# Kernel tuning notes

Measured on AMD Instinct MI355X. Metric: run time of the kernel, lower is better.

Reference implementation:

```python
import jax, jax.numpy as jnp
from jax import lax
import numpy as np

C = 16          # channel_n
HID = 128       # hidden_size
FIRE_RATE = 0.5
STEP_SIZE = 1.0
B, H, W = 16, 192, 192


def setup_inputs() -> dict:
    key = jax.random.key(0)
    ks = jax.random.split(key, 8)
    return {
        "x": jax.random.uniform(ks[0], (B, C, H, W), dtype=jnp.float32),
        "w1": jax.random.normal(ks[1], (HID, 3 * C), dtype=jnp.float32) * 0.1,
        "b1": jax.random.normal(ks[2], (HID,), dtype=jnp.float32) * 0.1,
        "w2": jax.random.normal(ks[3], (HID, HID), dtype=jnp.float32) * 0.1,
        "b2": jax.random.normal(ks[4], (HID,), dtype=jnp.float32) * 0.1,
        "w3": jax.random.normal(ks[5], (C, HID), dtype=jnp.float32) * 0.1,
        "b3": jax.random.normal(ks[6], (C,), dtype=jnp.float32) * 0.1,
        "fire_noise": jax.random.uniform(ks[7], (B, 1, H, W), dtype=jnp.float32),
    }


def _living_mask(x):
    # max_pool2d(alpha, 3, stride=1, pad=1) > 0.1 on alpha channel 3
    alpha = x[:, 3:4, :, :]
    m = lax.reduce_window(alpha, -jnp.inf, lax.max,
                          (1, 1, 3, 3), (1, 1, 1, 1), 'SAME')
    return m > 0.1


def _depthwise(x, k2d):
    # k2d: (3,3); depthwise conv over all C channels with same kernel
    kern = jnp.tile(k2d[None, None, :, :], (x.shape[1], 1, 1, 1))  # (C,1,3,3)
    return lax.conv_general_dilated(
        x, kern, window_strides=(1, 1), padding='SAME',
        feature_group_count=x.shape[1],
        dimension_numbers=('NCHW', 'OIHW', 'NCHW'))


def _relu6(x):
    return jnp.clip(x, 0.0, 6.0)


def reference(x, w1, b1, w2, b2, w3, b3, fire_noise):
    pre_life = _living_mask(x)

    # perceive: identity + sobel-x + sobel-y (angle = 0)
    sx = jnp.asarray(np.outer([1, 2, 1], [-1, 0, 1]) / 8.0, dtype=x.dtype)
    sy = sx.T
    y = jnp.concatenate([x, _depthwise(x, sx), _depthwise(x, sy)], axis=1)  # (B,3C,H,W)

    # pointwise MLP (1x1 convs) with ReLU6
    h = _relu6(jnp.einsum('bchw,oc->bohw', y, w1) + b1[None, :, None, None])
    h = _relu6(jnp.einsum('bchw,oc->bohw', h, w2) + b2[None, :, None, None])
    dx = (jnp.einsum('bchw,oc->bohw', h, w3) + b3[None, :, None, None]) * STEP_SIZE

    update_mask = (fire_noise <= FIRE_RATE).astype(x.dtype)  # (B,1,H,W)
    x_new = x + dx * update_mask

    post_life = _living_mask(x_new)
    life_mask = (pre_life & post_life).astype(x.dtype)
    return x_new * life_mask
```

## Files before the change

### kernel.cpp

```cpp
#include <hip/hip_runtime.h>

typedef _Float16 half8 __attribute__((ext_vector_type(8)));
typedef _Float16 half4 __attribute__((ext_vector_type(4)));
typedef float    f32x4 __attribute__((ext_vector_type(4)));

#define WH_HALVES      26624
#define ALPHA_BYTE_OFF 53248

#define NBLOCKS  256
#define ITERS    9

__global__ __launch_bounds__(256) void prep_weights(
    const float* __restrict__ w1, const float* __restrict__ w2,
    const float* __restrict__ w3, _Float16* __restrict__ wh)
{
    int i = blockIdx.x * 256 + threadIdx.x;
    if (i >= WH_HALVES) return;
    int rem = i & 511;
    int l = rem >> 3, j = rem & 7;
    int lr = l & 15, lg = l >> 4;
    _Float16 v;
    if (i < 8192) {
        int f = i >> 9;
        int nb = f >> 1, hh = f & 1;
        int o = nb * 16 + lr, k = hh * 32 + lg * 8 + j;
        v = (k < 48) ? (_Float16)w1[o * 48 + k] : (_Float16)0.f;
    } else if (i < 24576) {
        int f = (i - 8192) >> 9;
        int nb = f >> 2, kb = f & 3;
        v = (_Float16)w2[(nb * 16 + lr) * 128 + kb * 32 + lg * 8 + j];
    } else {
        int kb = (i - 24576) >> 9;
        v = (_Float16)w3[lr * 128 + kb * 32 + lg * 8 + j];
    }
    wh[i] = v;
}

#define HALO_UNITS 1584

__device__ __forceinline__ void halo_loads(const float* __restrict__ x,
                                           int bb, int h0, int w0, int tid,
                                           float pfv[2][4])
{
#pragma unroll
    for (int k = 0; k < 2; ++k) {
        int u = tid + k * 1024;
        bool valid = (u < HALO_UNITS);
        int uu = valid ? u : 0;
        int row = uu / 264, rem = uu % 264;
        int col = rem >> 2, cq = rem & 3;
        int hh = h0 - 1 + row, ww = w0 - 1 + col;
        bool inb = valid && hh >= 0 && hh < 192 && ww >= 0 && ww < 192;
#pragma unroll
        for (int cc = 0; cc < 4; ++cc)
            pfv[k][cc] = inb ? x[(((size_t)bb * 16 + cq * 4 + cc) * 192 + hh) * 192 + ww] : 0.f;
    }
}

__device__ __forceinline__ void halo_store(_Float16* __restrict__ dst, int tid,
                                           const float pfv[2][4])
{
#pragma unroll
    for (int k = 0; k < 2; ++k) {
        int u = tid + k * 1024;
        if (u < HALO_UNITS) {
            int row = u / 264, rem = u % 264;
            int col = rem >> 2, cq = rem & 3;
            half4 hv;
#pragma unroll
            for (int cc = 0; cc < 4; ++cc) hv[cc] = (_Float16)pfv[k][cc];
            *(half4*)&dst[(row * 66 + col) * 16 + cq * 4] = hv;
        }
    }
}

__global__ __launch_bounds__(1024, 4) void ca_main(
    const float* __restrict__ x,
    const float* __restrict__ b1g, const float* __restrict__ b2g,
    const float* __restrict__ b3g,
    const float* __restrict__ fire,
    const _Float16* __restrict__ wh,
    float* __restrict__ out,
    float* __restrict__ alpha_out)
{
    __shared__ __align__(16) struct {
        _Float16 w[WH_HALVES];
        _Float16 halo[2][6][66][16];
        _Float16 h[16][2048];
        float    b1[128], b2[128], b3[16];
    } s;

    const int tid  = threadIdx.x;
    const int lane = tid & 63;
    const int wave = tid >> 6;
    const int lr = lane & 15, hi = lane >> 4;

    {
        const uint4* src = (const uint4*)wh;
        uint4* dst = (uint4*)&s.w[0];
        for (int i = tid; i < 3328; i += 1024) dst[i] = src[i];
    }
    if (tid < 128) { s.b1[tid] = b1g[tid]; s.b2[tid] = b2g[tid]; }
    if (tid < 16)  { s.b3[tid] = b3g[tid]; }

    {
        int t = blockIdx.x;
        int bb = t / 144, rem = t % 144;
        int h0 = (rem / 3) * 4, w0 = (rem % 3) * 64;
        float pfv[2][4];
        halo_loads(x, bb, h0, w0, tid, pfv);
        halo_store(&s.halo[0][0][0][0], tid, pfv);
    }
    __syncthreads();

    const half8* wf = (const half8*)s.w;
    const int swzh = ((lr >> 1) & 7) << 4;
    char* hb = (char*)&s.h[wave][0];
    const int rowb = lr * 256;

    const int px = wave * 16 + lr;
    const int prow = px >> 6, pcol = px & 63;

    for (int it = 0; it < ITERS; ++it) {
        int t = blockIdx.x + it * NBLOCKS;
        int bb = t / 144, rem = t % 144;
        int h0 = (rem / 3) * 4, w0 = (rem % 3) * 64;
        const _Float16* hal = &s.halo[it & 1][0][0][0];

        float pfv[2][4];
        const bool have_next = (it + 1 < ITERS);
        if (have_next) {
            int tn = blockIdx.x + (it + 1) * NBLOCKS;
            int bbn = tn / 144, remn = tn % 144;
            halo_loads(x, bbn, (remn / 3) * 4, (remn % 3) * 64, tid, pfv);
        }
        const float fn = fire[(((size_t)bb) * 192 + h0 + prow) * 192 + w0 + pcol];

        half8 a1[2];
        {
            const half8 vz = { (_Float16)0.f, (_Float16)0.f, (_Float16)0.f, (_Float16)0.f,
                               (_Float16)0.f, (_Float16)0.f, (_Float16)0.f, (_Float16)0.f };
            half8 tp[3][3];
#pragma unroll
            for (int dr = 0; dr < 3; ++dr)
#pragma unroll
                for (int dc = 0; dc < 3; ++dc)
                    tp[dr][dc] = *(const half8*)&hal[((prow + dr) * 66 + pcol + dc) * 16 + (hi & 1) * 8];
            half8 gxa = (tp[0][2] - tp[0][0]) + (tp[2][2] - tp[2][0]);
            half8 gxb = (tp[1][2] - tp[1][0]);
            half8 gx  = gxa + gxb + gxb;
            half8 gya = (tp[2][0] - tp[0][0]) + (tp[2][2] - tp[0][2]);
            half8 gyb = (tp[2][1] - tp[0][1]);
            half8 gy  = gya + gyb + gyb;
            const _Float16 e = (_Float16)0.125f;
            gx = gx * e;
            gy = gy * e;
            a1[0] = (hi < 2) ? tp[1][1] : gx;
            a1[1] = (hi < 2) ? gy : vz;
        }

#pragma unroll
        for (int nb = 0; nb < 8; ++nb) {
            half8 bf0 = wf[(nb * 2    ) * 64 + lane];
            half8 bf1 = wf[(nb * 2 + 1) * 64 + lane];
            f32x4 acc = *(const f32x4*)&s.b1[nb * 16 + hi * 4];
            acc = __builtin_amdgcn_mfma_f32_16x16x32_f16(bf0, a1[0], acc, 0, 0, 0);
            acc = __builtin_amdgcn_mfma_f32_16x16x32_f16(bf1, a1[1], acc, 0, 0, 0);
            half4 hv;
#pragma unroll
            for (int rr = 0; rr < 4; ++rr)
                hv[rr] = (_Float16)fminf(fmaxf(acc[rr], 0.f), 6.f);
            *(half4*)(hb + rowb + ((nb * 32 + hi * 8) ^ swzh)) = hv;
        }

        half8 a2[4];
#pragma unroll
        for (int kb = 0; kb < 4; ++kb)
            a2[kb] = *(const half8*)(hb + rowb + ((kb * 64 + hi * 16) ^ swzh));
#pragma unroll
        for (int nb = 0; nb < 8; ++nb) {
            f32x4 acc = *(const f32x4*)&s.b2[nb * 16 + hi * 4];
#pragma unroll
            for (int kb = 0; kb < 4; ++kb) {
                half8 bf = wf[1024 + (nb * 4 + kb) * 64 + lane];
                acc = __builtin_amdgcn_mfma_f32_16x16x32_f16(bf, a2[kb], acc, 0, 0, 0);
            }
            half4 hv;
#pragma unroll
            for (int rr = 0; rr < 4; ++rr)
                hv[rr] = (_Float16)fminf(fmaxf(acc[rr], 0.f), 6.f);
            *(half4*)(hb + rowb + ((nb * 32 + hi * 8) ^ swzh)) = hv;
        }

        half8 a3[4];
#pragma unroll
        for (int kb = 0; kb < 4; ++kb)
            a3[kb] = *(const half8*)(hb + rowb + ((kb * 64 + hi * 16) ^ swzh));
        f32x4 acc3 = *(const f32x4*)&s.b3[hi * 4];
#pragma unroll
        for (int kb = 0; kb < 4; ++kb) {
            half8 bf = wf[3072 + kb * 64 + lane];
            acc3 = __builtin_amdgcn_mfma_f32_16x16x32_f16(bf, a3[kb], acc3, 0, 0, 0);
        }

        {
            half4 xq = *(const half4*)&hal[((1 + prow) * 66 + 1 + pcol) * 16 + hi * 4];
            const bool upd = (fn <= 0.5f);
            size_t obase = (((size_t)bb * 16) * 192 + h0 + prow) * 192 + w0 + pcol;
#pragma unroll
            for (int rr = 0; rr < 4; ++rr) {
                int c = hi * 4 + rr;
                float xn = (float)xq[rr] + (upd ? acc3[rr] : 0.f);
                out[obase + (size_t)c * 36864] = xn;
                if (hi == 0 && rr == 3)
                    alpha_out[(((size_t)bb) * 192 + h0 + prow) * 192 + w0 + pcol] = xn;
            }
        }

        if (have_next)
            halo_store(&s.halo[(it + 1) & 1][0][0][0], tid, pfv);
        __syncthreads();
    }
}

__global__ __launch_bounds__(256) void ca_mask(
    const float* __restrict__ x,
    const float* __restrict__ alpha_new,
    float* __restrict__ out)
{
    int pix = blockIdx.x * 256 + threadIdx.x;
    int ww = pix % 192; int t = pix / 192;
    int hh = t % 192;   int bb = t / 192;
    float pre = -1e30f, post = -1e30f;
#pragma unroll
    for (int di = -1; di <= 1; ++di) {
        int nh = hh + di;
        if (nh < 0 || nh >= 192) continue;
#pragma unroll
        for (int dj = -1; dj <= 1; ++dj) {
            int nw = ww + dj;
            if (nw < 0 || nw >= 192) continue;
            pre  = fmaxf(pre,  x[(((size_t)bb * 16 + 3) * 192 + nh) * 192 + nw]);
            post = fmaxf(post, alpha_new[(((size_t)bb) * 192 + nh) * 192 + nw]);
        }
    }
    bool alive = (pre > 0.1f) && (post > 0.1f);
    if (alive) return;
#pragma unroll
    for (int c = 0; c < 16; ++c) {
        out[(((size_t)bb * 16 + c) * 192 + hh) * 192 + ww] = 0.f;
    }
}

extern "C" void kernel_launch(void* const* d_in, const int* in_sizes, int n_in,
                              void* d_out, int out_size, void* d_ws, size_t ws_size,
                              hipStream_t stream) {
    const float* x    = (const float*)d_in[0];
    const float* w1   = (const float*)d_in[1];
    const float* b1   = (const float*)d_in[2];
    const float* w2   = (const float*)d_in[3];
    const float* b2   = (const float*)d_in[4];
    const float* w3   = (const float*)d_in[5];
    const float* b3   = (const float*)d_in[6];
    const float* fire = (const float*)d_in[7];
    float* out = (float*)d_out;

    _Float16* wh     = (_Float16*)d_ws;
    float* alpha_new = (float*)((char*)d_ws + ALPHA_BYTE_OFF);

    prep_weights<<<104, 256, 0, stream>>>(w1, w2, w3, wh);
    ca_main<<<NBLOCKS, 1024, 0, stream>>>(x, b1, b2, b3, fire, wh, out, alpha_new);
    ca_mask<<<2304, 256, 0, stream>>>(x, alpha_new, out);
}
```

Baseline: 73.47 us.

## Switch MLP to 32x32x16 MFMA with in-register permlane layer handoff

Measured after the change: 69.53 us. 1.06x faster.

```diff
diff --git a/kernel.cpp b/kernel.cpp
--- a/kernel.cpp
+++ b/kernel.cpp
@@ -1,14 +1,16 @@
 #include <hip/hip_runtime.h>
 
-typedef _Float16 half8 __attribute__((ext_vector_type(8)));
-typedef _Float16 half4 __attribute__((ext_vector_type(4)));
-typedef float    f32x4 __attribute__((ext_vector_type(4)));
+typedef _Float16 half8  __attribute__((ext_vector_type(8)));
+typedef _Float16 half4  __attribute__((ext_vector_type(4)));
+typedef _Float16 half2v __attribute__((ext_vector_type(2)));
+typedef float    f32x4  __attribute__((ext_vector_type(4)));
+typedef float    f32x16 __attribute__((ext_vector_type(16)));
 
 #define WH_HALVES      26624
 #define ALPHA_BYTE_OFF 53248
 
 #define NBLOCKS  256
-#define ITERS    9
+#define NTILES   1152
 
 __global__ __launch_bounds__(256) void prep_weights(
     const float* __restrict__ w1, const float* __restrict__ w2,
@@ -16,34 +18,31 @@
 {
     int i = blockIdx.x * 256 + threadIdx.x;
     if (i >= WH_HALVES) return;
-    int rem = i & 511;
+    int f = i >> 9, rem = i & 511;
     int l = rem >> 3, j = rem & 7;
-    int lr = l & 15, lg = l >> 4;
+    int l31 = l & 31, hi = l >> 5;
     _Float16 v;
-    if (i < 8192) {
-        int f = i >> 9;
-        int nb = f >> 1, hh = f & 1;
-        int o = nb * 16 + lr, k = hh * 32 + lg * 8 + j;
-        v = (k < 48) ? (_Float16)w1[o * 48 + k] : (_Float16)0.f;
-    } else if (i < 24576) {
-        int f = (i - 8192) >> 9;
-        int nb = f >> 2, kb = f & 3;
-        v = (_Float16)w2[(nb * 16 + lr) * 128 + kb * 32 + lg * 8 + j];
+    if (f < 12) {
+        int nb = f / 3, kb = f % 3;
+        v = (_Float16)w1[(nb * 32 + l31) * 48 + kb * 16 + hi * 8 + j];
+    } else if (f < 44) {
+        int ff = f - 12, nb = ff >> 3, kb = ff & 7;
+        v = (_Float16)w2[(nb * 32 + l31) * 128 + kb * 16 + hi * 8 + j];
     } else {
-        int kb = (i - 24576) >> 9;
-        v = (_Float16)w3[lr * 128 + kb * 32 + lg * 8 + j];
+        int kb = f - 44;
+        v = (l31 < 16) ? (_Float16)w3[l31 * 128 + kb * 16 + hi * 8 + j] : (_Float16)0.f;
     }
     wh[i] = v;
 }
 
-#define HALO_UNITS 1584
+#define HALO_UNITS 2640
 
 __device__ __forceinline__ void halo_loads(const float* __restrict__ x,
                                            int bb, int h0, int w0, int tid,
-                                           float pfv[2][4])
-{
-#pragma unroll
-    for (int k = 0; k < 2; ++k) {
+                                           float pfv[3][4])
+{
+#pragma unroll
+    for (int k = 0; k < 3; ++k) {
         int u = tid + k * 1024;
         bool valid = (u < HALO_UNITS);
         int uu = valid ? u : 0;
@@ -58,10 +57,10 @@
 }
 
 __device__ __forceinline__ void halo_store(_Float16* __restrict__ dst, int tid,
-                                           const float pfv[2][4])
-{
-#pragma unroll
-    for (int k = 0; k < 2; ++k) {
+                                           const float pfv[3][4])
+{
+#pragma unroll
+    for (int k = 0; k < 3; ++k) {
         int u = tid + k * 1024;
         if (u < HALO_UNITS) {
             int row = u / 264, rem = u % 264;
@@ -72,6 +71,26 @@
             *(half4*)&dst[(row * 66 + col) * 16 + cq * 4] = hv;
         }
     }
+}
+
+__device__ __forceinline__ void make_frags(const f32x16 acc, half8* fa, half8* fb)
+{
+    unsigned P[8];
+#pragma unroll
+    for (int w = 0; w < 8; ++w) {
+        half2v pk;
+        pk[0] = (_Float16)fminf(fmaxf(acc[2 * w    ], 0.f), 6.f);
+        pk[1] = (_Float16)fminf(fmaxf(acc[2 * w + 1], 0.f), 6.f);
+        P[w] = __builtin_bit_cast(unsigned, pk);
+    }
+    asm volatile("v_permlane32_swap_b32 %0, %1" : "+v"(P[0]), "+v"(P[2]));
+    asm volatile("v_permlane32_swap_b32 %0, %1" : "+v"(P[1]), "+v"(P[3]));
+    asm volatile("v_permlane32_swap_b32 %0, %1" : "+v"(P[4]), "+v"(P[6]));
+    asm volatile("v_permlane32_swap_b32 %0, %1" : "+v"(P[5]), "+v"(P[7]));
+    union { unsigned u[4]; half8 h; } A, B;
+    A.u[0] = P[0]; A.u[1] = P[1]; A.u[2] = P[2]; A.u[3] = P[3];
+    B.u[0] = P[4]; B.u[1] = P[5]; B.u[2] = P[6]; B.u[3] = P[7];
+    *fa = A.h; *fb = B.h;
 }
 
 __global__ __launch_bounds__(1024, 4) void ca_main(
@@ -85,67 +104,70 @@
 {
     __shared__ __align__(16) struct {
         _Float16 w[WH_HALVES];
-        _Float16 halo[2][6][66][16];
-        _Float16 h[16][2048];
-        float    b1[128], b2[128], b3[16];
+        _Float16 halo[2][10][66][16];
+        __align__(64) float b1d[4][2][16];
+        __align__(64) float b2d[4][2][16];
+        __align__(64) float b3d[2][16];
     } s;
 
     const int tid  = threadIdx.x;
     const int lane = tid & 63;
     const int wave = tid >> 6;
-    const int lr = lane & 15, hi = lane >> 4;
+    const int l31 = lane & 31, hi = lane >> 5;
 
     {
         const uint4* src = (const uint4*)wh;
         uint4* dst = (uint4*)&s.w[0];
         for (int i = tid; i < 3328; i += 1024) dst[i] = src[i];
     }
-    if (tid < 128) { s.b1[tid] = b1g[tid]; s.b2[tid] = b2g[tid]; }
-    if (tid < 16)  { s.b3[tid] = b3g[tid]; }
-
+    if (tid < 128) {
+        int o = tid, nb = o >> 5, ol = o & 31;
+        int r = (ol & 3) + 4 * (ol >> 3), hd = (ol >> 2) & 1;
+        s.b1d[nb][hd][r] = b1g[o];
+        s.b2d[nb][hd][r] = b2g[o];
+    }
+    if (tid < 32) {
+        int hd = tid >> 4, r = tid & 15;
+        s.b3d[hd][r] = (r < 8) ? b3g[(r & 3) + 8 * (r >> 2) + 4 * hd] : 0.f;
+    }
     {
         int t = blockIdx.x;
-        int bb = t / 144, rem = t % 144;
-        int h0 = (rem / 3) * 4, w0 = (rem % 3) * 64;
-        float pfv[2][4];
+        int bb = t / 72, rem = t % 72;
+        int h0 = (rem / 3) * 8, w0 = (rem % 3) * 64;
+        float pfv[3][4];
         halo_loads(x, bb, h0, w0, tid, pfv);
         halo_store(&s.halo[0][0][0][0], tid, pfv);
     }
     __syncthreads();
 
     const half8* wf = (const half8*)s.w;
-    const int swzh = ((lr >> 1) & 7) << 4;
-    char* hb = (char*)&s.h[wave][0];
-    const int rowb = lr * 256;
-
-    const int px = wave * 16 + lr;
+    const int px = wave * 32 + l31;
     const int prow = px >> 6, pcol = px & 63;
 
-    for (int it = 0; it < ITERS; ++it) {
+    for (int it = 0; ; ++it) {
         int t = blockIdx.x + it * NBLOCKS;
-        int bb = t / 144, rem = t % 144;
-        int h0 = (rem / 3) * 4, w0 = (rem % 3) * 64;
+        if (t >= NTILES) break;
+        int bb = t / 72, rem = t % 72;
+        int h0 = (rem / 3) * 8, w0 = (rem % 3) * 64;
         const _Float16* hal = &s.halo[it & 1][0][0][0];
 
-        float pfv[2][4];
-        const bool have_next = (it + 1 < ITERS);
+        float pfv[3][4];
+        int tn = t + NBLOCKS;
+        const bool have_next = (tn < NTILES);
         if (have_next) {
-            int tn = blockIdx.x + (it + 1) * NBLOCKS;
-            int bbn = tn / 144, remn = tn % 144;
-            halo_loads(x, bbn, (remn / 3) * 4, (remn % 3) * 64, tid, pfv);
+            int bbn = tn / 72, remn = tn % 72;
+            halo_loads(x, bbn, (remn / 3) * 8, (remn % 3) * 64, tid, pfv);
         }
         const float fn = fire[(((size_t)bb) * 192 + h0 + prow) * 192 + w0 + pcol];
 
-        half8 a1[2];
+        half8 bs0, bs1, bs2;
         {
-            const half8 vz = { (_Float16)0.f, (_Float16)0.f, (_Float16)0.f, (_Float16)0.f,
-                               (_Float16)0.f, (_Float16)0.f, (_Float16)0.f, (_Float16)0.f };
             half8 tp[3][3];
 #pragma unroll
             for (int dr = 0; dr < 3; ++dr)
 #pragma unroll
                 for (int dc = 0; dc < 3; ++dc)
-                    tp[dr][dc] = *(const half8*)&hal[((prow + dr) * 66 + pcol + dc) * 16 + (hi & 1) * 8];
+                    tp[dr][dc] = *(const half8*)&hal[((prow + dr) * 66 + pcol + dc) * 16 + hi * 8];
             half8 gxa = (tp[0][2] - tp[0][0]) + (tp[2][2] - tp[2][0]);
             half8 gxb = (tp[1][2] - tp[1][0]);
             half8 gx  = gxa + gxb + gxb;
@@ -153,66 +175,48 @@
             half8 gyb = (tp[2][1] - tp[0][1]);
             half8 gy  = gya + gyb + gyb;
             const _Float16 e = (_Float16)0.125f;
-            gx = gx * e;
-            gy = gy * e;
-            a1[0] = (hi < 2) ? tp[1][1] : gx;
-            a1[1] = (hi < 2) ? gy : vz;
-        }
-
-#pragma unroll
-        for (int nb = 0; nb < 8; ++nb) {
-            half8 bf0 = wf[(nb * 2    ) * 64 + lane];
-            half8 bf1 = wf[(nb * 2 + 1) * 64 + lane];
-            f32x4 acc = *(const f32x4*)&s.b1[nb * 16 + hi * 4];
-            acc = __builtin_amdgcn_mfma_f32_16x16x32_f16(bf0, a1[0], acc, 0, 0, 0);
-            acc = __builtin_amdgcn_mfma_f32_16x16x32_f16(bf1, a1[1], acc, 0, 0, 0);
-            half4 hv;
-#pragma unroll
-            for (int rr = 0; rr < 4; ++rr)
-                hv[rr] = (_Float16)fminf(fmaxf(acc[rr], 0.f), 6.f);
-            *(half4*)(hb + rowb + ((nb * 32 + hi * 8) ^ swzh)) = hv;
-        }
-
-        half8 a2[4];
-#pragma unroll
-        for (int kb = 0; kb < 4; ++kb)
-            a2[kb] = *(const half8*)(hb + rowb + ((kb * 64 + hi * 16) ^ swzh));
-#pragma unroll
-        for (int nb = 0; nb < 8; ++nb) {
-            f32x4 acc = *(const f32x4*)&s.b2[nb * 16 + hi * 4];
-#pragma unroll
-            for (int kb = 0; kb < 4; ++kb) {
-                half8 bf = wf[1024 + (nb * 4 + kb) * 64 + lane];
-                acc = __builtin_amdgcn_mfma_f32_16x16x32_f16(bf, a2[kb], acc, 0, 0, 0);
-            }
-            half4 hv;
-#pragma unroll
-            for (int rr = 0; rr < 4; ++rr)
-                hv[rr] = (_Float16)fminf(fmaxf(acc[rr], 0.f), 6.f);
-            *(half4*)(hb + rowb + ((nb * 32 + hi * 8) ^ swzh)) = hv;
-        }
-
-        half8 a3[4];
-#pragma unroll
-        for (int kb = 0; kb < 4; ++kb)
-            a3[kb] = *(const half8*)(hb + rowb + ((kb * 64 + hi * 16) ^ swzh));
-        f32x4 acc3 = *(const f32x4*)&s.b3[hi * 4];
-#pragma unroll
-        for (int kb = 0; kb < 4; ++kb) {
-            half8 bf = wf[3072 + kb * 64 + lane];
-            acc3 = __builtin_amdgcn_mfma_f32_16x16x32_f16(bf, a3[kb], acc3, 0, 0, 0);
-        }
+            bs0 = tp[1][1];
+            bs1 = gx * e;
+            bs2 = gy * e;
+        }
+
+        half8 l2b[8];
+#pragma unroll
+        for (int nb = 0; nb < 4; ++nb) {
+            f32x16 acc = *(const f32x16*)&s.b1d[nb][hi][0];
+            acc = __builtin_amdgcn_mfma_f32_32x32x16_f16(wf[(nb * 3 + 0) * 64 + lane], bs0, acc, 0, 0, 0);
+            acc = __builtin_amdgcn_mfma_f32_32x32x16_f16(wf[(nb * 3 + 1) * 64 + lane], bs1, acc, 0, 0, 0);
+            acc = __builtin_amdgcn_mfma_f32_32x32x16_f16(wf[(nb * 3 + 2) * 64 + lane], bs2, acc, 0, 0, 0);
+            make_frags(acc, &l2b[2 * nb], &l2b[2 * nb + 1]);
+        }
+
+        half8 l3b[8];
+#pragma unroll
+        for (int nb = 0; nb < 4; ++nb) {
+            f32x16 acc = *(const f32x16*)&s.b2d[nb][hi][0];
+#pragma unroll
+            for (int kb = 0; kb < 8; ++kb)
+                acc = __builtin_amdgcn_mfma_f32_32x32x16_f16(wf[(12 + nb * 8 + kb) * 64 + lane], l2b[kb], acc, 0, 0, 0);
+            make_frags(acc, &l3b[2 * nb], &l3b[2 * nb + 1]);
+        }
+
+        f32x16 acc3 = *(const f32x16*)&s.b3d[hi][0];
+#pragma unroll
+        for (int kb = 0; kb < 8; ++kb)
+            acc3 = __builtin_amdgcn_mfma_f32_32x32x16_f16(wf[(44 + kb) * 64 + lane], l3b[kb], acc3, 0, 0, 0);
 
         {
-            half4 xq = *(const half4*)&hal[((1 + prow) * 66 + 1 + pcol) * 16 + hi * 4];
+            half4 xq0 = *(const half4*)&hal[((1 + prow) * 66 + 1 + pcol) * 16 + hi * 4];
+            half4 xq1 = *(const half4*)&hal[((1 + prow) * 66 + 1 + pcol) * 16 + 8 + hi * 4];
             const bool upd = (fn <= 0.5f);
             size_t obase = (((size_t)bb * 16) * 192 + h0 + prow) * 192 + w0 + pcol;
 #pragma unroll
-            for (int rr = 0; rr < 4; ++rr) {
-                int c = hi * 4 + rr;
-                float xn = (float)xq[rr] + (upd ? acc3[rr] : 0.f);
+            for (int r = 0; r < 8; ++r) {
+                int c = (r & 3) + 8 * (r >> 2) + 4 * hi;
+                float xc = (float)((r < 4) ? xq0[r & 3] : xq1[r & 3]);
+                float xn = xc + (upd ? acc3[r] : 0.f);
                 out[obase + (size_t)c * 36864] = xn;
-                if (hi == 0 && rr == 3)
+                if (hi == 0 && r == 3)
                     alpha_out[(((size_t)bb) * 192 + h0 + prow) * 192 + w0 + pcol] = xn;
             }
         }
```
